# Kernel optimization log

Hardware: AMD Instinct MI355X
Metric: run time of the kernel (lower is better)

## Reference

```python
import jax, jax.numpy as jnp
import numpy as np

NUM_GROUPS = 8
NUM_HEADS = 4
EPS = 1e-5


def group_norm(x, w, b):
    # x: [B, C, H, W]; normalize over (C/G, H, W) within each of G groups
    B, C, H, W = x.shape
    xg = x.reshape(B, NUM_GROUPS, C // NUM_GROUPS, H, W)
    mean = xg.mean(axis=(2, 3, 4), keepdims=True)
    var = xg.var(axis=(2, 3, 4), keepdims=True)
    xn = ((xg - mean) * jax.lax.rsqrt(var + EPS)).reshape(B, C, H, W)
    return xn * w[None, :, None, None] + b[None, :, None, None]


def setup_inputs() -> dict:
    key = jax.random.key(0)
    ks = jax.random.split(key, 7)
    B, C, H, W = 4, 256, 64, 64
    x = jax.random.normal(ks[0], (B, C, H, W), dtype=jnp.float32)
    gn_w = jax.random.normal(ks[1], (C,), dtype=jnp.float32) * 0.1 + 1.0
    gn_b = jax.random.normal(ks[2], (C,), dtype=jnp.float32) * 0.1
    qkv_w = jax.random.normal(ks[3], (3 * C, C), dtype=jnp.float32) / np.sqrt(C)
    qkv_b = jax.random.normal(ks[4], (3 * C,), dtype=jnp.float32) * 0.02
    proj_w = jax.random.normal(ks[5], (C, C), dtype=jnp.float32) / np.sqrt(C)
    proj_b = jax.random.normal(ks[6], (C,), dtype=jnp.float32) * 0.02
    return {"x": x, "gn_w": gn_w, "gn_b": gn_b, "qkv_w": qkv_w,
            "qkv_b": qkv_b, "proj_w": proj_w, "proj_b": proj_b}


def reference(x, gn_w, gn_b, qkv_w, qkv_b, proj_w, proj_b):
    B, C, H, W = x.shape
    nh = NUM_HEADS
    hd = C // nh
    scale = hd ** -0.5
    N = H * W

    h = group_norm(x, gn_w, gn_b)
    # 1x1 conv == channel matmul: [B, 3C, H, W]
    qkv = jnp.einsum('oc,bchw->bohw', qkv_w, h) + qkv_b[None, :, None, None]
    qkv = qkv.reshape(B, 3, nh, hd, N)  # matches torch .view(B,3,nh,hd,HW)
    q, k, v = qkv[:, 0], qkv[:, 1], qkv[:, 2]  # each [B, nh, hd, N]

    attn = jnp.einsum('bhdn,bhdm->bhnm', q, k) * scale  # [B, nh, N, N]
    attn = jax.nn.softmax(attn, axis=-1)
    out = jnp.einsum('bhnm,bhdm->bhdn', attn, v)  # [B, nh, hd, N]
    out = out.reshape(B, C, H, W)

    proj = jnp.einsum('oc,bchw->bohw', proj_w, out) + proj_b[None, :, None, None]
    return x + proj
```

## Files before the change

kernel.cpp:

```cpp
#include <hip/hip_runtime.h>
#include <hip/hip_bf16.h>

#define BB   4
#define CC   256
#define NN   4096
#define NH   4
#define HD   64
#define NG   8
#define GSZ  32
#define EPSV 1e-5f
#define SCALE_L2E 0.18033688f

typedef __bf16 bf16x8 __attribute__((ext_vector_type(8)));
typedef float  f32x4  __attribute__((ext_vector_type(4)));

#define MFMA16(a, b, c)  __builtin_amdgcn_mfma_f32_16x16x32_bf16((a), (b), (c), 0, 0, 0)

#if __has_builtin(__builtin_amdgcn_exp2f)
#define EXP2F __builtin_amdgcn_exp2f
#else
#define EXP2F exp2f
#endif

__device__ inline unsigned short f2bf(float f) {
    unsigned int u = __float_as_uint(f);
    u += 0x7fffu + ((u >> 16) & 1u);
    return (unsigned short)(u >> 16);
}

__device__ __forceinline__ bf16x8 pk8(const f32x4& p0, const f32x4& p1) {
    alignas(16) unsigned int u[4];
    u[0] = __builtin_amdgcn_perm(__float_as_uint(p0[1]), __float_as_uint(p0[0]), 0x07060302u);
    u[1] = __builtin_amdgcn_perm(__float_as_uint(p0[3]), __float_as_uint(p0[2]), 0x07060302u);
    u[2] = __builtin_amdgcn_perm(__float_as_uint(p1[1]), __float_as_uint(p1[0]), 0x07060302u);
    u[3] = __builtin_amdgcn_perm(__float_as_uint(p1[3]), __float_as_uint(p1[2]), 0x07060302u);
    return *reinterpret_cast<bf16x8*>(u);
}

__device__ __forceinline__ void async_ld16(void* lds, const void* g) {
    __builtin_amdgcn_global_load_lds(
        (const __attribute__((address_space(1))) unsigned int*)g,
        (__attribute__((address_space(3))) unsigned int*)lds, 16, 0, 0);
}

__global__ void k_prep(const float* __restrict__ x, float* __restrict__ stats,
                       const float* __restrict__ wq, const float* __restrict__ wp,
                       unsigned short* __restrict__ oq, unsigned short* __restrict__ op) {
    int blk = blockIdx.x;
    int t = threadIdx.x;
    if (blk >= 256) {
        int i = (blk - 256) * 256 + t;
        if (i < 3 * CC * CC) oq[i] = f2bf(wq[i]);
        if (i < CC * CC)     op[i] = f2bf(wp[i]);
        return;
    }
    int b = blk >> 6, g = (blk >> 3) & 7, s = blk & 7;
    const float* p = x + ((size_t)(b * CC + g * GSZ)) * NN + s * 16384;
    float s0 = 0.f, s1 = 0.f;
    #pragma unroll
    for (int i = 0; i < 64; ++i) { float v = p[i * 256 + t]; s0 += v; s1 += v * v; }
    #pragma unroll
    for (int m = 1; m <= 32; m <<= 1) { s0 += __shfl_xor(s0, m); s1 += __shfl_xor(s1, m); }
    __shared__ float ls[8];
    int w = t >> 6;
    if ((t & 63) == 0) { ls[w * 2] = s0; ls[w * 2 + 1] = s1; }
    __syncthreads();
    if (t == 0) {
        float a0 = ls[0] + ls[2] + ls[4] + ls[6];
        float a1 = ls[1] + ls[3] + ls[5] + ls[7];
        atomicAdd(&stats[(b * NG + g) * 2 + 0], a0);
        atomicAdd(&stats[(b * NG + g) * 2 + 1], a1);
    }
}

__global__ void k_gnapply(const float* __restrict__ x, const float* __restrict__ gw,
                          const float* __restrict__ gb, const float* __restrict__ stats,
                          unsigned short* __restrict__ ht) {
    int b = blockIdx.z, ct = blockIdx.y, nt = blockIdx.x;
    int c0 = ct * 32, n0 = nt * 64;
    int t = threadIdx.x;
    __shared__ float tile[32][65];
    const float* xp = x + ((size_t)(b * CC + c0)) * NN + n0;
    int cl = t >> 6, nl = t & 63;
    #pragma unroll
    for (int p = 0; p < 8; ++p)
        tile[p * 4 + cl][nl] = xp[(size_t)(p * 4 + cl) * NN + nl];
    float sum = stats[(b * NG + ct) * 2 + 0];
    float ssq = stats[(b * NG + ct) * 2 + 1];
    float mean = sum * (1.0f / 131072.0f);
    float var  = ssq * (1.0f / 131072.0f) - mean * mean;
    float inv  = rsqrtf(var + EPSV);
    __syncthreads();
    int nw = t >> 2, ci = (t & 3) * 8;
    alignas(16) unsigned short o8[8];
    #pragma unroll
    for (int j = 0; j < 8; ++j) {
        int c = c0 + ci + j;
        float v = (tile[ci + j][nw] - mean) * inv * gw[c] + gb[c];
        o8[j] = f2bf(v);
    }
    *reinterpret_cast<uint4*>(ht + ((size_t)(b * NN + n0 + nw)) * CC + c0 + ci) =
        *reinterpret_cast<const uint4*>(o8);
}

__global__ void __launch_bounds__(256)
k_qkv(const unsigned short* __restrict__ ht, const unsigned short* __restrict__ wq,
      const float* __restrict__ qb,
      unsigned short* __restrict__ qt, unsigned short* __restrict__ kt,
      unsigned short* __restrict__ vt) {
    int bx = blockIdx.x, by = blockIdx.y;
    int t = threadIdx.x, wave = t >> 6, lane = t & 63;
    int l15 = lane & 15, quad = lane >> 4;
    int wm = wave >> 1, wn = wave & 1;

    __shared__ alignas(16) unsigned char At[2][8192];
    __shared__ alignas(16) unsigned char Bt[2][8192];

    const char* Ag = (const char*)wq + (size_t)by * 65536;
    const char* Bg = (const char*)ht + (size_t)bx * 65536;
    int row0 = t >> 2, slot = t & 3;
    size_t a0 = (size_t)row0 * 512 + slot * 16;
    size_t a1 = a0 + 64 * 512;
    unsigned int dst0 = wave * 1024;

    auto stage = [&](int buf, int kk) {
        size_t ko = (size_t)kk * 64;
        async_ld16(At[buf] + dst0,        Ag + a0 + ko);
        async_ld16(At[buf] + 4096 + dst0, Ag + a1 + ko);
        async_ld16(Bt[buf] + dst0,        Bg + a0 + ko);
        async_ld16(Bt[buf] + 4096 + dst0, Bg + a1 + ko);
    };

    f32x4 acc[4][4];
    #pragma unroll
    for (int i = 0; i < 4; ++i)
        #pragma unroll
        for (int j = 0; j < 4; ++j) acc[i][j] = (f32x4){0.f, 0.f, 0.f, 0.f};

    stage(0, 0);
    __syncthreads();

    for (int kk = 0; kk < 8; ++kk) {
        int cur = kk & 1;
        if (kk < 7) stage(cur ^ 1, kk + 1);
        bf16x8 af[4], bf[4];
        #pragma unroll
        for (int f = 0; f < 4; ++f) {
            af[f] = *reinterpret_cast<const bf16x8*>(At[cur] + (wm * 64 + f * 16 + l15) * 64 + quad * 16);
            bf[f] = *reinterpret_cast<const bf16x8*>(Bt[cur] + (wn * 64 + f * 16 + l15) * 64 + quad * 16);
        }
        #pragma unroll
        for (int fm = 0; fm < 4; ++fm)
            #pragma unroll
            for (int fn = 0; fn < 4; ++fn)
                acc[fm][fn] = MFMA16(af[fm], bf[fn], acc[fm][fn]);
        __syncthreads();
    }

    int s = by >> 1;
    int nn0 = bx * 128;
    int b = nn0 >> 12, nbase = nn0 & 4095;
    #pragma unroll
    for (int fm = 0; fm < 4; ++fm) {
        int o = by * 128 + wm * 64 + fm * 16 + quad * 4;
        int h = (o >> 6) & 3, d0 = o & 63;
        float bias[4];
        #pragma unroll
        for (int r = 0; r < 4; ++r) bias[r] = qb[o + r];
        #pragma unroll
        for (int fn = 0; fn < 4; ++fn) {
            int n = nbase + wn * 64 + fn * 16 + l15;
            if (s == 0) {
                alignas(8) unsigned short o4[4];
                #pragma unroll
                for (int r = 0; r < 4; ++r) o4[r] = f2bf((acc[fm][fn][r] + bias[r]) * SCALE_L2E);
                *reinterpret_cast<uint2*>(qt + (((size_t)(b * NH + h) * NN) + n) * HD + d0) =
                    *reinterpret_cast<const uint2*>(o4);
            } else if (s == 1) {
                alignas(8) unsigned short o4[4];
                #pragma unroll
                for (int r = 0; r < 4; ++r) o4[r] = f2bf(acc[fm][fn][r] + bias[r]);
                *reinterpret_cast<uint2*>(kt + (((size_t)(b * NH + h) * NN) + n) * HD + d0) =
                    *reinterpret_cast<const uint2*>(o4);
            } else {
                int cl = n & 31;
                int pn = (n & ~31) | (((cl & 12) << 1) | ((cl >> 4) << 2) | (cl & 3));
                #pragma unroll
                for (int r = 0; r < 4; ++r)
                    vt[((size_t)(b * NH + h) * HD + d0 + r) * NN + pn] = f2bf(acc[fm][fn][r] + bias[r]);
            }
        }
    }
}

__global__ void __launch_bounds__(256, 4)
k_attn(const unsigned short* __restrict__ qt, const unsigned short* __restrict__ kt,
       const unsigned short* __restrict__ vt,
       unsigned short* __restrict__ op0, unsigned short* __restrict__ op1,
       float* __restrict__ lip) {
    int bh = blockIdx.y;
    int split = blockIdx.z;
    int t = threadIdx.x, wave = t >> 6, lane = t & 63;
    int l15 = lane & 15, quad = lane >> 4;
    int qbase = blockIdx.x * 128 + wave * 32;
    int kbase = split * 2048;
    const unsigned short* qp = qt + (size_t)bh * NN * HD;
    const unsigned short* kp = kt + (size_t)bh * NN * HD;
    const unsigned short* vp = vt + (size_t)bh * HD * NN;

    __shared__ alignas(16) unsigned char kbuf[2][8192];
    __shared__ alignas(16) unsigned char vbuf[2][8192];

    int lr8 = lane >> 3, lc8 = lane & 7;
    int swz = lc8 ^ lr8;
    const char* ksrc = (const char*)kp + (size_t)(kbase + wave * 16 + lr8) * 128 + swz * 16;
    const char* vsrc = (const char*)vp + (size_t)(wave * 16 + lr8) * 8192 + (size_t)kbase * 2 + swz * 16;
    unsigned int dstw = wave * 2048;

    auto stage = [&](int buf) {
        async_ld16(kbuf[buf] + dstw,        ksrc);
        async_ld16(kbuf[buf] + dstw + 1024, ksrc + 1024);
        ksrc += 8192;
        async_ld16(vbuf[buf] + dstw,        vsrc);
        async_ld16(vbuf[buf] + dstw + 1024, vsrc + 8 * 8192);
        vsrc += 128;
    };

    bf16x8 qaA0 = *reinterpret_cast<const bf16x8*>(qp + (size_t)(qbase + l15) * HD + quad * 8);
    bf16x8 qaA1 = *reinterpret_cast<const bf16x8*>(qp + (size_t)(qbase + l15) * HD + 32 + quad * 8);
    bf16x8 qaB0 = *reinterpret_cast<const bf16x8*>(qp + (size_t)(qbase + 16 + l15) * HD + quad * 8);
    bf16x8 qaB1 = *reinterpret_cast<const bf16x8*>(qp + (size_t)(qbase + 16 + l15) * HD + 32 + quad * 8);

    f32x4 OA[4], OB[4];
    #pragma unroll
    for (int i = 0; i < 4; ++i) { OA[i] = (f32x4){0.f, 0.f, 0.f, 0.f}; OB[i] = (f32x4){0.f, 0.f, 0.f, 0.f}; }
    float liA = 0.f, liB = 0.f;

    int sx = l15 & 7;

    auto compute = [&](const unsigned char* kb, const unsigned char* vbb) {
        f32x4 sA0[2], sA1[2], sB0[2], sB1[2];
        #pragma unroll
        for (int s = 0; s < 2; ++s) {
            int r0 = (s * 32 + l15) * 128;
            bf16x8 k00 = *reinterpret_cast<const bf16x8*>(kb + r0 + ((quad ^ sx) * 16));
            bf16x8 k01 = *reinterpret_cast<const bf16x8*>(kb + r0 + (((quad + 4) ^ sx) * 16));
            bf16x8 k10 = *reinterpret_cast<const bf16x8*>(kb + r0 + 2048 + ((quad ^ sx) * 16));
            bf16x8 k11 = *reinterpret_cast<const bf16x8*>(kb + r0 + 2048 + (((quad + 4) ^ sx) * 16));
            sA0[s] = (f32x4){0.f,0.f,0.f,0.f};  sA1[s] = (f32x4){0.f,0.f,0.f,0.f};
            sB0[s] = (f32x4){0.f,0.f,0.f,0.f};  sB1[s] = (f32x4){0.f,0.f,0.f,0.f};
            sA0[s] = MFMA16(k00, qaA0, sA0[s]);  sA0[s] = MFMA16(k01, qaA1, sA0[s]);
            sA1[s] = MFMA16(k10, qaA0, sA1[s]);  sA1[s] = MFMA16(k11, qaA1, sA1[s]);
            sB0[s] = MFMA16(k00, qaB0, sB0[s]);  sB0[s] = MFMA16(k01, qaB1, sB0[s]);
            sB1[s] = MFMA16(k10, qaB0, sB1[s]);  sB1[s] = MFMA16(k11, qaB1, sB1[s]);
        }
        #pragma unroll
        for (int s = 0; s < 2; ++s) {
            f32x4 pA0, pA1, pB0, pB1;
            #pragma unroll
            for (int r = 0; r < 4; ++r) {
                pA0[r] = EXP2F(sA0[s][r]);  pA1[r] = EXP2F(sA1[s][r]);
                pB0[r] = EXP2F(sB0[s][r]);  pB1[r] = EXP2F(sB1[s][r]);
            }
            liA += (pA0[0] + pA0[1] + pA0[2] + pA0[3]) + (pA1[0] + pA1[1] + pA1[2] + pA1[3]);
            liB += (pB0[0] + pB0[1] + pB0[2] + pB0[3]) + (pB1[0] + pB1[1] + pB1[2] + pB1[3]);

            bf16x8 fA = pk8(pA0, pA1);
            bf16x8 fB = pk8(pB0, pB1);

            #pragma unroll
            for (int dc = 0; dc < 4; ++dc) {
                const unsigned char* vrow = vbb + (dc * 16 + l15) * 128;
                bf16x8 vv = *reinterpret_cast<const bf16x8*>(vrow + (((s * 4 + quad) ^ sx) * 16));
                OA[dc] = MFMA16(fA, vv, OA[dc]);
                OB[dc] = MFMA16(fB, vv, OB[dc]);
            }
        }
    };

    stage(0);
    __syncthreads();

    for (int p = 0; p < 16; ++p) {
        stage(1);
        compute(kbuf[0], vbuf[0]);
        __syncthreads();
        if (p < 15) stage(0);
        compute(kbuf[1], vbuf[1]);
        __syncthreads();
    }

    liA += __shfl_xor(liA, 16);  liA += __shfl_xor(liA, 32);
    liB += __shfl_xor(liB, 16);  liB += __shfl_xor(liB, 32);

    unsigned short* op = split ? op1 : op0;
    int b = bh >> 2, h = bh & 3;
    #pragma unroll
    for (int dc = 0; dc < 4; ++dc) {
        #pragma unroll
        for (int r = 0; r < 4; ++r) {
            int qA = qbase + quad * 4 + r;
            op[((size_t)(b * NN) + qA) * CC + h * HD + dc * 16 + l15]      = f2bf(OA[dc][r]);
            op[((size_t)(b * NN) + qA + 16) * CC + h * HD + dc * 16 + l15] = f2bf(OB[dc][r]);
        }
    }
    float* lp = lip + (size_t)split * (16 * NN) + (size_t)bh * NN + qbase;
    if (quad == 0)      lp[l15]      = liA;
    else if (quad == 1) lp[16 + l15] = liB;
}

__global__ void __launch_bounds__(256)
k_comb(unsigned short* ao, const unsigned short* __restrict__ p1, const float* __restrict__ lip) {
    int g = blockIdx.x * 256 + threadIdx.x;
    int d8 = g & 7;
    int h  = (g >> 3) & 3;
    int n  = (g >> 5) & 4095;
    int b  = g >> 17;
    int bh = b * 4 + h;
    float li0 = lip[(size_t)bh * NN + n];
    float li1 = lip[(size_t)16 * NN + (size_t)bh * NN + n];
    float inv = 1.0f / (li0 + li1);
    size_t idx = ((size_t)(b * NN) + n) * CC + h * HD + d8 * 8;
    uint4 u0 = *reinterpret_cast<const uint4*>(ao + idx);
    uint4 u1 = *reinterpret_cast<const uint4*>(p1 + idx);
    const unsigned short* a0 = reinterpret_cast<const unsigned short*>(&u0);
    const unsigned short* a1 = reinterpret_cast<const unsigned short*>(&u1);
    alignas(16) unsigned short o8[8];
    #pragma unroll
    for (int i = 0; i < 8; ++i) {
        float f0 = __uint_as_float((unsigned)a0[i] << 16);
        float f1 = __uint_as_float((unsigned)a1[i] << 16);
        o8[i] = f2bf((f0 + f1) * inv);
    }
    *reinterpret_cast<uint4*>(ao + idx) = *reinterpret_cast<const uint4*>(o8);
}

__global__ void __launch_bounds__(256)
k_proj(const unsigned short* __restrict__ ao, const unsigned short* __restrict__ wp,
       const float* __restrict__ pb, const float* __restrict__ x,
       float* __restrict__ out) {
    int bx = blockIdx.x, by = blockIdx.y;
    int t = threadIdx.x, wave = t >> 6, lane = t & 63;
    int l15 = lane & 15, quad = lane >> 4;
    int wm = wave >> 1, wn = wave & 1;

    __shared__ alignas(16) unsigned char At[2][4096];
    __shared__ alignas(16) unsigned char Bt[2][4096];

    const char* Ag = (const char*)wp + (size_t)by * 32768;
    const char* Bg = (const char*)ao + (size_t)bx * 32768;
    int row0 = t >> 2, slot = t & 3;
    size_t a0 = (size_t)row0 * 512 + slot * 16;
    unsigned int dst0 = wave * 1024;

    auto stage = [&](int buf, int kk) {
        size_t ko = (size_t)kk * 64;
        async_ld16(At[buf] + dst0, Ag + a0 + ko);
        async_ld16(Bt[buf] + dst0, Bg + a0 + ko);
    };

    f32x4 acc[2][2];
    #pragma unroll
    for (int i = 0; i < 2; ++i)
        #pragma unroll
        for (int j = 0; j < 2; ++j) acc[i][j] = (f32x4){0.f, 0.f, 0.f, 0.f};

    stage(0, 0);
    __syncthreads();

    for (int kk = 0; kk < 8; ++kk) {
        int cur = kk & 1;
        if (kk < 7) stage(cur ^ 1, kk + 1);
        bf16x8 af[2], bf[2];
        #pragma unroll
        for (int f = 0; f < 2; ++f) {
            af[f] = *reinterpret_cast<const bf16x8*>(At[cur] + (wm * 32 + f * 16 + l15) * 64 + quad * 16);
            bf[f] = *reinterpret_cast<const bf16x8*>(Bt[cur] + (wn * 32 + f * 16 + l15) * 64 + quad * 16);
        }
        #pragma unroll
        for (int fm = 0; fm < 2; ++fm)
            #pragma unroll
            for (int fn = 0; fn < 2; ++fn)
                acc[fm][fn] = MFMA16(af[fm], bf[fn], acc[fm][fn]);
        __syncthreads();
    }

    int nn0 = bx * 64;
    int b = nn0 >> 12, nbase = nn0 & 4095;
    #pragma unroll
    for (int fm = 0; fm < 2; ++fm) {
        int o = by * 64 + wm * 32 + fm * 16 + quad * 4;
        float bias[4];
        #pragma unroll
        for (int r = 0; r < 4; ++r) bias[r] = pb[o + r];
        #pragma unroll
        for (int fn = 0; fn < 2; ++fn) {
            int n = nbase + wn * 32 + fn * 16 + l15;
            #pragma unroll
            for (int r = 0; r < 4; ++r) {
                size_t idx = ((size_t)(b * CC + o + r)) * NN + n;
                out[idx] = acc[fm][fn][r] + bias[r] + x[idx];
            }
        }
    }
}

extern "C" void kernel_launch(void* const* d_in, const int* in_sizes, int n_in,
                              void* d_out, int out_size, void* d_ws, size_t ws_size,
                              hipStream_t stream) {
    const float* x     = (const float*)d_in[0];
    const float* gw    = (const float*)d_in[1];
    const float* gb    = (const float*)d_in[2];
    const float* qkvw  = (const float*)d_in[3];
    const float* qkvb  = (const float*)d_in[4];
    const float* projw = (const float*)d_in[5];
    const float* projb = (const float*)d_in[6];
    float* out = (float*)d_out;

    char* w = (char*)d_ws;
    size_t off = 0;
    unsigned short* ht = (unsigned short*)(w + off); off += (size_t)BB * NN * CC * 2;
    unsigned short* qt = (unsigned short*)(w + off); off += (size_t)BB * NH * NN * HD * 2;
    unsigned short* kt = (unsigned short*)(w + off); off += (size_t)BB * NH * NN * HD * 2;
    unsigned short* vt = (unsigned short*)(w + off); off += (size_t)BB * NH * HD * NN * 2;
    unsigned short* ao = (unsigned short*)(w + off); off += (size_t)BB * NN * CC * 2;
    unsigned short* wqb = (unsigned short*)(w + off); off += (size_t)3 * CC * CC * 2;
    unsigned short* wpb = (unsigned short*)(w + off); off += (size_t)CC * CC * 2;
    float* stats = (float*)(w + off); off += BB * NG * 2 * sizeof(float);
    float* lip   = (float*)(w + off); off += (size_t)2 * 16 * NN * sizeof(float);

    hipMemsetAsync(stats, 0, BB * NG * 2 * sizeof(float), stream);
    k_prep<<<1024, 256, 0, stream>>>(x, stats, qkvw, projw, wqb, wpb);
    k_gnapply<<<dim3(NN / 64, CC / 32, BB), 256, 0, stream>>>(x, gw, gb, stats, ht);
    k_qkv<<<dim3(BB * NN / 128, 6), 256, 0, stream>>>(ht, wqb, qkvb, qt, kt, vt);
    k_attn<<<dim3(NN / 128, BB * NH, 2), 256, 0, stream>>>(qt, kt, vt, ao, ht, lip);
    k_comb<<<2048, 256, 0, stream>>>(ao, ht, lip);
    k_proj<<<dim3(BB * NN / 64, CC / 64), 256, 0, stream>>>(ao, wpb, projb, x, out);
}
```

Measured before the change: 190.0 us.

## Stage V output through LDS for coalesced stores; compute row sums via MFMA

In the QKV kernel, the V-slice epilogue now writes results into a padded shared tile and then emits 16-byte coalesced stores in the permuted layout, replacing scattered 2-byte global writes. In the attention kernel, softmax row sums are accumulated with an extra MFMA against a vector of ones instead of scalar adds plus cross-lane shuffles. The first QK MFMA now takes the zero accumulator directly. The trade-off is added LDS traffic and a barrier in the V epilogue, two extra MFMAs per step, and row sums accumulated from bf16-rounded probabilities.

```diff
diff --git a/kernel.cpp b/kernel.cpp
--- a/kernel.cpp
+++ b/kernel.cpp
@@ -113,8 +113,7 @@
     int l15 = lane & 15, quad = lane >> 4;
     int wm = wave >> 1, wn = wave & 1;
 
-    __shared__ alignas(16) unsigned char At[2][8192];
-    __shared__ alignas(16) unsigned char Bt[2][8192];
+    __shared__ alignas(16) unsigned char smem[33792];
 
     const char* Ag = (const char*)wq + (size_t)by * 65536;
     const char* Bg = (const char*)ht + (size_t)bx * 65536;
@@ -125,10 +124,12 @@
 
     auto stage = [&](int buf, int kk) {
         size_t ko = (size_t)kk * 64;
-        async_ld16(At[buf] + dst0,        Ag + a0 + ko);
-        async_ld16(At[buf] + 4096 + dst0, Ag + a1 + ko);
-        async_ld16(Bt[buf] + dst0,        Bg + a0 + ko);
-        async_ld16(Bt[buf] + 4096 + dst0, Bg + a1 + ko);
+        unsigned char* Ab = smem + buf * 8192;
+        unsigned char* Bb = smem + 16384 + buf * 8192;
+        async_ld16(Ab + dst0,        Ag + a0 + ko);
+        async_ld16(Ab + 4096 + dst0, Ag + a1 + ko);
+        async_ld16(Bb + dst0,        Bg + a0 + ko);
+        async_ld16(Bb + 4096 + dst0, Bg + a1 + ko);
     };
 
     f32x4 acc[4][4];
@@ -146,8 +147,8 @@
         bf16x8 af[4], bf[4];
         #pragma unroll
         for (int f = 0; f < 4; ++f) {
-            af[f] = *reinterpret_cast<const bf16x8*>(At[cur] + (wm * 64 + f * 16 + l15) * 64 + quad * 16);
-            bf[f] = *reinterpret_cast<const bf16x8*>(Bt[cur] + (wn * 64 + f * 16 + l15) * 64 + quad * 16);
+            af[f] = *reinterpret_cast<const bf16x8*>(smem + cur * 8192 + (wm * 64 + f * 16 + l15) * 64 + quad * 16);
+            bf[f] = *reinterpret_cast<const bf16x8*>(smem + 16384 + cur * 8192 + (wn * 64 + f * 16 + l15) * 64 + quad * 16);
         }
         #pragma unroll
         for (int fm = 0; fm < 4; ++fm)
@@ -160,35 +161,61 @@
     int s = by >> 1;
     int nn0 = bx * 128;
     int b = nn0 >> 12, nbase = nn0 & 4095;
-    #pragma unroll
-    for (int fm = 0; fm < 4; ++fm) {
-        int o = by * 128 + wm * 64 + fm * 16 + quad * 4;
-        int h = (o >> 6) & 3, d0 = o & 63;
-        float bias[4];
-        #pragma unroll
-        for (int r = 0; r < 4; ++r) bias[r] = qb[o + r];
-        #pragma unroll
-        for (int fn = 0; fn < 4; ++fn) {
-            int n = nbase + wn * 64 + fn * 16 + l15;
-            if (s == 0) {
+    if (s < 2) {
+        #pragma unroll
+        for (int fm = 0; fm < 4; ++fm) {
+            int o = by * 128 + wm * 64 + fm * 16 + quad * 4;
+            int h = (o >> 6) & 3, d0 = o & 63;
+            float bias[4];
+            #pragma unroll
+            for (int r = 0; r < 4; ++r) bias[r] = qb[o + r];
+            #pragma unroll
+            for (int fn = 0; fn < 4; ++fn) {
+                int n = nbase + wn * 64 + fn * 16 + l15;
                 alignas(8) unsigned short o4[4];
-                #pragma unroll
-                for (int r = 0; r < 4; ++r) o4[r] = f2bf((acc[fm][fn][r] + bias[r]) * SCALE_L2E);
-                *reinterpret_cast<uint2*>(qt + (((size_t)(b * NH + h) * NN) + n) * HD + d0) =
-                    *reinterpret_cast<const uint2*>(o4);
-            } else if (s == 1) {
-                alignas(8) unsigned short o4[4];
-                #pragma unroll
-                for (int r = 0; r < 4; ++r) o4[r] = f2bf(acc[fm][fn][r] + bias[r]);
-                *reinterpret_cast<uint2*>(kt + (((size_t)(b * NH + h) * NN) + n) * HD + d0) =
-                    *reinterpret_cast<const uint2*>(o4);
-            } else {
-                int cl = n & 31;
-                int pn = (n & ~31) | (((cl & 12) << 1) | ((cl >> 4) << 2) | (cl & 3));
+                if (s == 0) {
+                    #pragma unroll
+                    for (int r = 0; r < 4; ++r) o4[r] = f2bf((acc[fm][fn][r] + bias[r]) * SCALE_L2E);
+                    *reinterpret_cast<uint2*>(qt + (((size_t)(b * NH + h) * NN) + n) * HD + d0) =
+                        *reinterpret_cast<const uint2*>(o4);
+                } else {
+                    #pragma unroll
+                    for (int r = 0; r < 4; ++r) o4[r] = f2bf(acc[fm][fn][r] + bias[r]);
+                    *reinterpret_cast<uint2*>(kt + (((size_t)(b * NH + h) * NN) + n) * HD + d0) =
+                        *reinterpret_cast<const uint2*>(o4);
+                }
+            }
+        }
+    } else {
+        unsigned short* vtile = (unsigned short*)smem;
+        #pragma unroll
+        for (int fm = 0; fm < 4; ++fm) {
+            int o  = by * 128 + wm * 64 + fm * 16 + quad * 4;
+            int ol = wm * 64 + fm * 16 + quad * 4;
+            float bias[4];
+            #pragma unroll
+            for (int r = 0; r < 4; ++r) bias[r] = qb[o + r];
+            #pragma unroll
+            for (int fn = 0; fn < 4; ++fn) {
+                int nl = wn * 64 + fn * 16 + l15;
                 #pragma unroll
                 for (int r = 0; r < 4; ++r)
-                    vt[((size_t)(b * NH + h) * HD + d0 + r) * NN + pn] = f2bf(acc[fm][fn][r] + bias[r]);
+                    vtile[(ol + r) * 132 + nl] = f2bf(acc[fm][fn][r] + bias[r]);
             }
+        }
+        __syncthreads();
+        int hbase = (by - 4) * 2;
+        #pragma unroll
+        for (int pass = 0; pass < 8; ++pass) {
+            int row  = pass * 16 + (t >> 4);
+            int col0 = (t & 15) * 8;
+            int nb = (col0 & ~31) | ((col0 & 16) >> 1) | ((col0 & 8) >> 1);
+            const unsigned short* src = vtile + row * 132 + nb;
+            uint2 lo = *reinterpret_cast<const uint2*>(src);
+            uint2 hi = *reinterpret_cast<const uint2*>(src + 16);
+            uint4 o4 = make_uint4(lo.x, lo.y, hi.x, hi.y);
+            int h = hbase + (row >> 6), d = row & 63;
+            *reinterpret_cast<uint4*>(vt + ((size_t)(b * NH + h) * HD + d) * NN + nbase + col0) = o4;
         }
     }
 }
@@ -231,10 +258,15 @@
     bf16x8 qaB0 = *reinterpret_cast<const bf16x8*>(qp + (size_t)(qbase + 16 + l15) * HD + quad * 8);
     bf16x8 qaB1 = *reinterpret_cast<const bf16x8*>(qp + (size_t)(qbase + 16 + l15) * HD + 32 + quad * 8);
 
+    const f32x4 Z4 = (f32x4){0.f, 0.f, 0.f, 0.f};
+    bf16x8 vone;
+    #pragma unroll
+    for (int i = 0; i < 8; ++i) vone[i] = (__bf16)1.0f;
+
     f32x4 OA[4], OB[4];
     #pragma unroll
-    for (int i = 0; i < 4; ++i) { OA[i] = (f32x4){0.f, 0.f, 0.f, 0.f}; OB[i] = (f32x4){0.f, 0.f, 0.f, 0.f}; }
-    float liA = 0.f, liB = 0.f;
+    for (int i = 0; i < 4; ++i) { OA[i] = Z4; OB[i] = Z4; }
+    f32x4 liAA = Z4, liBB = Z4;
 
     int sx = l15 & 7;
 
@@ -247,12 +279,10 @@
             bf16x8 k01 = *reinterpret_cast<const bf16x8*>(kb + r0 + (((quad + 4) ^ sx) * 16));
             bf16x8 k10 = *reinterpret_cast<const bf16x8*>(kb + r0 + 2048 + ((quad ^ sx) * 16));
             bf16x8 k11 = *reinterpret_cast<const bf16x8*>(kb + r0 + 2048 + (((quad + 4) ^ sx) * 16));
-            sA0[s] = (f32x4){0.f,0.f,0.f,0.f};  sA1[s] = (f32x4){0.f,0.f,0.f,0.f};
-            sB0[s] = (f32x4){0.f,0.f,0.f,0.f};  sB1[s] = (f32x4){0.f,0.f,0.f,0.f};
-            sA0[s] = MFMA16(k00, qaA0, sA0[s]);  sA0[s] = MFMA16(k01, qaA1, sA0[s]);
-            sA1[s] = MFMA16(k10, qaA0, sA1[s]);  sA1[s] = MFMA16(k11, qaA1, sA1[s]);
-            sB0[s] = MFMA16(k00, qaB0, sB0[s]);  sB0[s] = MFMA16(k01, qaB1, sB0[s]);
-            sB1[s] = MFMA16(k10, qaB0, sB1[s]);  sB1[s] = MFMA16(k11, qaB1, sB1[s]);
+            sA0[s] = MFMA16(k00, qaA0, Z4);  sA0[s] = MFMA16(k01, qaA1, sA0[s]);
+            sA1[s] = MFMA16(k10, qaA0, Z4);  sA1[s] = MFMA16(k11, qaA1, sA1[s]);
+            sB0[s] = MFMA16(k00, qaB0, Z4);  sB0[s] = MFMA16(k01, qaB1, sB0[s]);
+            sB1[s] = MFMA16(k10, qaB0, Z4);  sB1[s] = MFMA16(k11, qaB1, sB1[s]);
         }
         #pragma unroll
         for (int s = 0; s < 2; ++s) {
@@ -262,11 +292,11 @@
                 pA0[r] = EXP2F(sA0[s][r]);  pA1[r] = EXP2F(sA1[s][r]);
                 pB0[r] = EXP2F(sB0[s][r]);  pB1[r] = EXP2F(sB1[s][r]);
             }
-            liA += (pA0[0] + pA0[1] + pA0[2] + pA0[3]) + (pA1[0] + pA1[1] + pA1[2] + pA1[3]);
-            liB += (pB0[0] + pB0[1] + pB0[2] + pB0[3]) + (pB1[0] + pB1[1] + pB1[2] + pB1[3]);
-
             bf16x8 fA = pk8(pA0, pA1);
             bf16x8 fB = pk8(pB0, pB1);
+
+            liAA = MFMA16(fA, vone, liAA);
+            liBB = MFMA16(fB, vone, liBB);
 
             #pragma unroll
             for (int dc = 0; dc < 4; ++dc) {
@@ -290,9 +320,6 @@
         __syncthreads();
     }
 
-    liA += __shfl_xor(liA, 16);  liA += __shfl_xor(liA, 32);
-    liB += __shfl_xor(liB, 16);  liB += __shfl_xor(liB, 32);
-
     unsigned short* op = split ? op1 : op0;
     int b = bh >> 2, h = bh & 3;
     #pragma unroll
@@ -305,8 +332,13 @@
         }
     }
     float* lp = lip + (size_t)split * (16 * NN) + (size_t)bh * NN + qbase;
-    if (quad == 0)      lp[l15]      = liA;
-    else if (quad == 1) lp[16 + l15] = liB;
+    if (l15 == 0) {
+        #pragma unroll
+        for (int r = 0; r < 4; ++r) {
+            lp[quad * 4 + r]      = liAA[r];
+            lp[16 + quad * 4 + r] = liBB[r];
+        }
+    }
 }
 
 __global__ void __launch_bounds__(256)
```

Measured after the change: 188.7 us. No clear change (-0.7%).
